# Performance work log

Measured on AMD Instinct MI355X. Metric: run time of the kernel, lower is better.

The kernel has to match this reference:

```python
import jax, jax.numpy as jnp
import numpy as np

TOPK = 5
EPS = 1e-8  # torch CosineSimilarity eps


def setup_inputs() -> dict:
    key = jax.random.key(0)
    k1, k2, k3 = jax.random.split(key, 3)
    B, N, D, L = 64, 100000, 768, 32
    query = jax.random.normal(k1, (B, D), dtype=jnp.float32)
    knowledge_embed = jax.random.normal(k2, (N, D), dtype=jnp.float32)
    knowledge_full = jax.random.randint(k3, (N, L), 0, 30000, dtype=jnp.int32)
    return {"query": query, "knowledge_embed": knowledge_embed, "knowledge_full": knowledge_full}


def reference(query, knowledge_embed, knowledge_full):
    # Batched cosine similarity: [B, N]
    q_norm = jnp.linalg.norm(query, axis=-1, keepdims=True)            # [B, 1]
    k_norm = jnp.linalg.norm(knowledge_embed, axis=-1, keepdims=True)  # [N, 1]
    dots = jnp.einsum("bd,nd->bn", query, knowledge_embed)             # [B, N]
    denom = jnp.maximum(q_norm * k_norm.T, EPS)                        # [B, N]
    sims = dots / denom
    # topk over knowledge axis
    _, indices = jax.lax.top_k(sims, TOPK)                             # [B, topk]
    topk_embed = knowledge_embed[indices]                              # [B, topk, D]
    topk_knowledge = knowledge_full[indices]                           # [B, topk, L]
    return (topk_knowledge, topk_embed)
```

## Files before the change

kernel.cpp:

```cpp
#include <hip/hip_runtime.h>
#include <cfloat>
#include <climits>


#define BQ 64
#define DD 768
#define NK 100000
#define LK 32
#define K_TOP 5
#define TROWS 16
#define NTIL (NK / TROWS)
#define NBLKS 512
#define T_CAND 16

typedef __attribute__((ext_vector_type(8))) short short8;
typedef __attribute__((ext_vector_type(4))) float f32x4;

static __device__ __forceinline__ ushort bf16_rtn(float x) {
    uint u = __float_as_uint(x);
    return (ushort)((u + 0x7FFFu + ((u >> 16) & 1u)) >> 16);
}

#define INS8(v, n, va, ia)                                                  \
    _Pragma("unroll")                                                       \
    for (int m_ = 0; m_ < 8; ++m_) {                                        \
        if ((v) > va[m_]) {                                                 \
            float tv_ = va[m_]; va[m_] = (v); (v) = tv_;                    \
            int ti_ = ia[m_]; ia[m_] = (n); (n) = ti_;                      \
        }                                                                   \
    }

__global__ __launch_bounds__(256) void prep_kernel(const float* __restrict__ q,
                                                   ushort* __restrict__ qf,
                                                   float* __restrict__ qn) {
    const int b = blockIdx.x, t = threadIdx.x;
    __shared__ float red[4];
    float v[3];
    float s = 0.f;
#pragma unroll
    for (int i = 0; i < 3; ++i) {
        v[i] = q[b * DD + t + i * 256];
        s = fmaf(v[i], v[i], s);
    }
    for (int off = 32; off > 0; off >>= 1) s += __shfl_down(s, off, 64);
    if ((t & 63) == 0) red[t >> 6] = s;
    __syncthreads();
    const float tot = red[0] + red[1] + red[2] + red[3];
    const float rq = rsqrtf(tot);
    const int qb = b >> 4, bi = b & 15;
#pragma unroll
    for (int i = 0; i < 3; ++i) {
        const int k = t + i * 256;
        const int kt = k >> 5, lg = (k >> 3) & 3, j = k & 7;
        qf[((size_t)(kt * 4 + qb) * 64 + lg * 16 + bi) * 8 + j] = bf16_rtn(v[i] * rq);
    }
    if (t == 0) qn[b] = sqrtf(tot);
}

__global__ __launch_bounds__(256) void sims_kernel(const ushort* __restrict__ qf,
                                                   const float* __restrict__ ke,
                                                   float2* __restrict__ pv) {
    __shared__ ushort Bb[2][TROWS * DD];
    __shared__ float  S[BQ][17];

    const int t = threadIdx.x;
    const int w = t >> 6, l = t & 63;
    const int lg = l >> 4, li = l & 15;
    const int qd = t & 63, jq = t >> 6;

    float v8[8]; int i8[8];
#pragma unroll
    for (int m = 0; m < 8; ++m) { v8[m] = -FLT_MAX; i8[m] = INT_MAX; }

    f32x4 sr[4][3];
    int tile = blockIdx.x;

    {
        const float* g = ke + (size_t)(tile * TROWS + w * 4) * DD + l * 4;
#pragma unroll
        for (int i = 0; i < 4; ++i)
#pragma unroll
            for (int c = 0; c < 3; ++c)
                sr[i][c] = *(const f32x4*)(g + i * DD + c * 256);
    }

    int cur = 0;
    while (true) {
        const int nxt = tile + NBLKS;

        char* bb = (char*)(&Bb[cur][0]);
#pragma unroll
        for (int i = 0; i < 4; ++i) {
            float s = 0.f;
#pragma unroll
            for (int c = 0; c < 3; ++c)
#pragma unroll
                for (int j = 0; j < 4; ++j) s = fmaf(sr[i][c][j], sr[i][c][j], s);
#pragma unroll
            for (int off = 1; off < 64; off <<= 1) s += __shfl_xor(s, off, 64);
            const float rk = rsqrtf(s);
            const int row = w * 4 + i;
            const int base = row * 1536 + l * 8;
            const int sw = (row & 7) << 4;
#pragma unroll
            for (int c = 0; c < 3; ++c) {
                ushort4 u = make_ushort4(bf16_rtn(sr[i][c][0] * rk),
                                         bf16_rtn(sr[i][c][1] * rk),
                                         bf16_rtn(sr[i][c][2] * rk),
                                         bf16_rtn(sr[i][c][3] * rk));
                *(ushort4*)(bb + ((base + c * 512) ^ sw)) = u;
            }
        }
        if (nxt < NTIL) {
            const float* g = ke + (size_t)(nxt * TROWS + w * 4) * DD + l * 4;
#pragma unroll
            for (int i = 0; i < 4; ++i)
#pragma unroll
                for (int c = 0; c < 3; ++c)
                    sr[i][c] = *(const f32x4*)(g + i * DD + c * 256);
        }
        asm volatile("s_waitcnt lgkmcnt(0)" ::: "memory");
        __builtin_amdgcn_sched_barrier(0);
        __builtin_amdgcn_s_barrier();
        __builtin_amdgcn_sched_barrier(0);

        const ushort* aq = qf + (size_t)w * 512 + l * 8;
        const int boff = li * 1536 + lg * 16;
        const int bsw = (li & 7) << 4;
        f32x4 acc = (f32x4){0.f, 0.f, 0.f, 0.f};
        short8 a[4], br[2];
        a[0] = *(const short8*)(aq);
        a[1] = *(const short8*)(aq + 2048);
        a[2] = *(const short8*)(aq + 4096);
        br[0] = *(const short8*)(bb + (boff ^ bsw));
#pragma unroll
        for (int kt = 0; kt < 24; ++kt) {
            const int ca = kt & 3, cb = kt & 1;
            if (kt < 21) a[(kt + 3) & 3] = *(const short8*)(aq + (kt + 3) * 2048);
            if (kt < 23)
                br[cb ^ 1] = *(const short8*)(bb + ((boff + (kt + 1) * 64) ^ bsw));
            acc = __builtin_amdgcn_mfma_f32_16x16x32_bf16(a[ca], br[cb], acc, 0, 0, 0);
        }

#pragma unroll
        for (int r = 0; r < 4; ++r) S[w * 16 + lg * 4 + r][li] = acc[r];
        asm volatile("s_waitcnt lgkmcnt(0)" ::: "memory");
        __builtin_amdgcn_sched_barrier(0);
        __builtin_amdgcn_s_barrier();
        __builtin_amdgcn_sched_barrier(0);

        {
            const int nb = tile * TROWS + jq * 4;
#pragma unroll
            for (int j = 0; j < 4; ++j) {
                float v = S[qd][jq * 4 + j]; int n = nb + j;
                INS8(v, n, v8, i8);
            }
        }
        if (nxt >= NTIL) break;
        tile = nxt; cur ^= 1;
    }

    __syncthreads();
    float2* mg = (float2*)(&Bb[0][0]);
#pragma unroll
    for (int m = 0; m < 8; ++m) mg[t * 8 + m] = make_float2(v8[m], __int_as_float(i8[m]));
    __syncthreads();
    if (t < BQ) {
        float vf[8]; int nf[8];
#pragma unroll
        for (int m = 0; m < 8; ++m) { vf[m] = -FLT_MAX; nf[m] = INT_MAX; }
        for (int s = 0; s < 4; ++s) {
            const float2* rowp = &mg[(t + s * 64) * 8];
#pragma unroll
            for (int m = 0; m < 8; ++m) {
                float v = rowp[m].x; int n = __float_as_int(rowp[m].y);
                INS8(v, n, vf, nf);
            }
        }
        float2* dst = pv + ((size_t)t * NBLKS + blockIdx.x) * 8;
#pragma unroll
        for (int m = 0; m < 8; ++m) dst[m] = make_float2(vf[m], __int_as_float(nf[m]));
    }
}

__global__ __launch_bounds__(256) void merge_rescore_kernel(
    const float2* __restrict__ pv,
    const float* __restrict__ q, const float* __restrict__ ke,
    const int* __restrict__ kf, const float* __restrict__ qn,
    float* __restrict__ out) {
    const int qi = blockIdx.x, t = threadIdx.x;
    __shared__ float sv[256][8];
    __shared__ int   si[256][8];
    __shared__ int   ci[T_CAND];
    __shared__ float cs_[T_CAND];
    __shared__ int   fi[K_TOP];

    float v8[8]; int i8[8];
#pragma unroll
    for (int m = 0; m < 8; ++m) { v8[m] = -FLT_MAX; i8[m] = INT_MAX; }

    const float2* src = pv + (size_t)qi * NBLKS * 8;
#pragma unroll 4
    for (int c = t; c < NBLKS * 8; c += 256) {
        float2 e = src[c];
        float v = e.x; int n = __float_as_int(e.y);
        INS8(v, n, v8, i8);
    }
#pragma unroll
    for (int m = 0; m < 8; ++m) { sv[t][m] = v8[m]; si[t][m] = i8[m]; }
    __syncthreads();

    for (int active = 64; active >= 4; active >>= 2) {
        if (t < active) {
#pragma unroll
            for (int m = 0; m < 8; ++m) { v8[m] = -FLT_MAX; i8[m] = INT_MAX; }
            for (int s = 0; s < 4; ++s) {
                int row = t * 4 + s;
#pragma unroll
                for (int m = 0; m < 8; ++m) {
                    float v = sv[row][m]; int n = si[row][m];
                    INS8(v, n, v8, i8);
                }
            }
        }
        __syncthreads();
        if (t < active) {
#pragma unroll
            for (int m = 0; m < 8; ++m) { sv[t][m] = v8[m]; si[t][m] = i8[m]; }
        }
        __syncthreads();
    }

    if (t == 0) {
        float v16[T_CAND]; int i16[T_CAND];
#pragma unroll
        for (int m = 0; m < T_CAND; ++m) { v16[m] = -FLT_MAX; i16[m] = INT_MAX; }
        for (int row = 0; row < 4; ++row) {
#pragma unroll
            for (int m = 0; m < 8; ++m) {
                float v = sv[row][m]; int n = si[row][m];
#pragma unroll
                for (int p = 0; p < T_CAND; ++p) {
                    if (v > v16[p]) {
                        float tv = v16[p]; v16[p] = v; v = tv;
                        int ti = i16[p]; i16[p] = n; n = ti;
                    }
                }
            }
        }
#pragma unroll
        for (int m = 0; m < T_CAND; ++m) ci[m] = i16[m];
    }
    __syncthreads();

    {
        const int w = t >> 6, lane = t & 63;
        for (int cc = 0; cc < 4; ++cc) {
            int c = w * 4 + cc;
            int row = ci[c];
            const float* kp = ke + (size_t)row * DD + lane * 12;
            const float* qp = q + qi * DD + lane * 12;
            float d = 0.f, ks = 0.f;
#pragma unroll
            for (int i = 0; i < 12; ++i) {
                float kv = kp[i];
                d = fmaf(qp[i], kv, d);
                ks = fmaf(kv, kv, ks);
            }
#pragma unroll
            for (int off = 32; off > 0; off >>= 1) {
                d += __shfl_xor(d, off, 64);
                ks += __shfl_xor(ks, off, 64);
            }
            if (lane == 0)
                cs_[c] = d / fmaxf(qn[qi] * sqrtf(ks), 1e-8f);
        }
    }
    __syncthreads();

    if (t == 0) {
        float v5[K_TOP]; int i5[K_TOP];
#pragma unroll
        for (int m = 0; m < K_TOP; ++m) { v5[m] = -FLT_MAX; i5[m] = INT_MAX; }
        for (int c = 0; c < T_CAND; ++c) {
            float v = cs_[c]; int n = ci[c];
#pragma unroll
            for (int m = 0; m < K_TOP; ++m) {
                bool take = (v > v5[m]) || (v == v5[m] && n < i5[m]);
                if (take) {
                    float tv = v5[m]; v5[m] = v; v = tv;
                    int ti = i5[m]; i5[m] = n; n = ti;
                }
            }
        }
#pragma unroll
        for (int m = 0; m < K_TOP; ++m) fi[m] = i5[m];
    }
    __syncthreads();

    for (int pos = t; pos < K_TOP * LK; pos += 256) {
        int m = pos >> 5, lgi = pos & 31;
        out[(qi * K_TOP + m) * LK + lgi] = (float)kf[(size_t)fi[m] * LK + lgi];
    }
    const int EO = BQ * K_TOP * LK;
    for (int m = 0; m < K_TOP; ++m) {
        const float4* srcp = (const float4*)(ke + (size_t)fi[m] * DD);
        float4* dstp = (float4*)(out + EO + (size_t)(qi * K_TOP + m) * DD);
        for (int pos = t; pos < DD / 4; pos += 256) dstp[pos] = srcp[pos];
    }
}

extern "C" void kernel_launch(void* const* d_in, const int* in_sizes, int n_in,
                              void* d_out, int out_size, void* d_ws, size_t ws_size,
                              hipStream_t stream) {
    const float* query = (const float*)d_in[0];
    const float* ke    = (const float*)d_in[1];
    const int*   kf    = (const int*)d_in[2];
    float* out = (float*)d_out;

    float2* pv = (float2*)d_ws;
    ushort* qf = (ushort*)((char*)d_ws + (size_t)BQ * NBLKS * 8 * sizeof(float2));
    float*  qn = (float*)((char*)qf + (size_t)24 * 4 * 64 * 8 * sizeof(ushort));

    prep_kernel<<<BQ, 256, 0, stream>>>(query, qf, qn);
    sims_kernel<<<NBLKS, 256, 0, stream>>>(qf, ke, pv);
    merge_rescore_kernel<<<BQ, 256, 0, stream>>>(pv, query, ke, kf, qn, out);
}
```

Baseline: 172.2 us.

## Give each wave its own key tile, converting to bf16 in registers without LDS staging

The sims kernel now assigns one 16-row key tile to each wavefront instead of one per block. Each wave loads fp32 key rows straight into registers, packs them to bf16 by truncation with a byte permute, and accumulates the squared norm as it goes, so the LDS double buffer and the block barriers disappear. The query is stored row-major in bf16 and read from global/L2 per wave, and the grid grows to 768 blocks. The cost is more query reloads from global memory and truncating rather than round-to-nearest bf16 conversion for keys, which the rescore stage has to absorb.

```diff
diff --git a/kernel.cpp b/kernel.cpp
--- a/kernel.cpp
+++ b/kernel.cpp
@@ -10,7 +10,8 @@
 #define K_TOP 5
 #define TROWS 16
 #define NTIL (NK / TROWS)
-#define NBLKS 512
+#define NBLK 768
+#define NWAV (NBLK * 4)
 #define T_CAND 16
 
 typedef __attribute__((ext_vector_type(8))) short short8;
@@ -31,7 +32,7 @@
     }
 
 __global__ __launch_bounds__(256) void prep_kernel(const float* __restrict__ q,
-                                                   ushort* __restrict__ qf,
+                                                   ushort* __restrict__ qbf,
                                                    float* __restrict__ qn) {
     const int b = blockIdx.x, t = threadIdx.x;
     __shared__ float red[4];
@@ -47,122 +48,99 @@
     __syncthreads();
     const float tot = red[0] + red[1] + red[2] + red[3];
     const float rq = rsqrtf(tot);
-    const int qb = b >> 4, bi = b & 15;
-#pragma unroll
-    for (int i = 0; i < 3; ++i) {
-        const int k = t + i * 256;
-        const int kt = k >> 5, lg = (k >> 3) & 3, j = k & 7;
-        qf[((size_t)(kt * 4 + qb) * 64 + lg * 16 + bi) * 8 + j] = bf16_rtn(v[i] * rq);
-    }
+#pragma unroll
+    for (int i = 0; i < 3; ++i)
+        qbf[b * DD + t + i * 256] = bf16_rtn(v[i] * rq);
     if (t == 0) qn[b] = sqrtf(tot);
 }
 
-__global__ __launch_bounds__(256) void sims_kernel(const ushort* __restrict__ qf,
+__global__ __launch_bounds__(256) void sims_kernel(const ushort* __restrict__ qbf,
                                                    const float* __restrict__ ke,
                                                    float2* __restrict__ pv) {
-    __shared__ ushort Bb[2][TROWS * DD];
-    __shared__ float  S[BQ][17];
+    __shared__ float  S[4][BQ][17];
+    __shared__ float2 mg[256 * 8];
 
     const int t = threadIdx.x;
     const int w = t >> 6, l = t & 63;
     const int lg = l >> 4, li = l & 15;
-    const int qd = t & 63, jq = t >> 6;
 
     float v8[8]; int i8[8];
 #pragma unroll
     for (int m = 0; m < 8; ++m) { v8[m] = -FLT_MAX; i8[m] = INT_MAX; }
 
-    f32x4 sr[4][3];
-    int tile = blockIdx.x;
-
-    {
-        const float* g = ke + (size_t)(tile * TROWS + w * 4) * DD + l * 4;
-#pragma unroll
-        for (int i = 0; i < 4; ++i)
-#pragma unroll
-            for (int c = 0; c < 3; ++c)
-                sr[i][c] = *(const f32x4*)(g + i * DD + c * 256);
-    }
-
-    int cur = 0;
-    while (true) {
-        const int nxt = tile + NBLKS;
-
-        char* bb = (char*)(&Bb[cur][0]);
-#pragma unroll
-        for (int i = 0; i < 4; ++i) {
-            float s = 0.f;
-#pragma unroll
-            for (int c = 0; c < 3; ++c)
-#pragma unroll
-                for (int j = 0; j < 4; ++j) s = fmaf(sr[i][c][j], sr[i][c][j], s);
-#pragma unroll
-            for (int off = 1; off < 64; off <<= 1) s += __shfl_xor(s, off, 64);
-            const float rk = rsqrtf(s);
-            const int row = w * 4 + i;
-            const int base = row * 1536 + l * 8;
-            const int sw = (row & 7) << 4;
-#pragma unroll
-            for (int c = 0; c < 3; ++c) {
-                ushort4 u = make_ushort4(bf16_rtn(sr[i][c][0] * rk),
-                                         bf16_rtn(sr[i][c][1] * rk),
-                                         bf16_rtn(sr[i][c][2] * rk),
-                                         bf16_rtn(sr[i][c][3] * rk));
-                *(ushort4*)(bb + ((base + c * 512) ^ sw)) = u;
-            }
-        }
-        if (nxt < NTIL) {
-            const float* g = ke + (size_t)(nxt * TROWS + w * 4) * DD + l * 4;
-#pragma unroll
-            for (int i = 0; i < 4; ++i)
-#pragma unroll
-                for (int c = 0; c < 3; ++c)
-                    sr[i][c] = *(const f32x4*)(g + i * DD + c * 256);
-        }
-        asm volatile("s_waitcnt lgkmcnt(0)" ::: "memory");
-        __builtin_amdgcn_sched_barrier(0);
-        __builtin_amdgcn_s_barrier();
-        __builtin_amdgcn_sched_barrier(0);
-
-        const ushort* aq = qf + (size_t)w * 512 + l * 8;
-        const int boff = li * 1536 + lg * 16;
-        const int bsw = (li & 7) << 4;
-        f32x4 acc = (f32x4){0.f, 0.f, 0.f, 0.f};
-        short8 a[4], br[2];
-        a[0] = *(const short8*)(aq);
-        a[1] = *(const short8*)(aq + 2048);
-        a[2] = *(const short8*)(aq + 4096);
-        br[0] = *(const short8*)(bb + (boff ^ bsw));
+    const ushort* abase = qbf + (size_t)li * DD + lg * 8;
+
+    const int gw = blockIdx.x * 4 + w;
+    for (int tile = gw; tile < NTIL; tile += NWAV) {
+        const int n0 = tile * TROWS;
+        const float* bbase = ke + (size_t)(n0 + li) * DD + lg * 8;
+
+        f32x4  br[4][2];
+        short8 ar[2][4];
+
+#pragma unroll
+        for (int p = 0; p < 4; ++p) {
+            br[p][0] = *(const f32x4*)(bbase + p * 32);
+            br[p][1] = *(const f32x4*)(bbase + p * 32 + 4);
+        }
+#pragma unroll
+        for (int s = 0; s < 2; ++s)
+#pragma unroll
+            for (int g = 0; g < 4; ++g)
+                ar[s][g] = *(const short8*)(abase + (size_t)g * 16 * DD + s * 32);
+
+        f32x4 acc[4];
+#pragma unroll
+        for (int g = 0; g < 4; ++g) acc[g] = (f32x4){0.f, 0.f, 0.f, 0.f};
+        float bsq = 0.f;
+
 #pragma unroll
         for (int kt = 0; kt < 24; ++kt) {
-            const int ca = kt & 3, cb = kt & 1;
-            if (kt < 21) a[(kt + 3) & 3] = *(const short8*)(aq + (kt + 3) * 2048);
-            if (kt < 23)
-                br[cb ^ 1] = *(const short8*)(bb + ((boff + (kt + 1) * 64) ^ bsw));
-            acc = __builtin_amdgcn_mfma_f32_16x16x32_bf16(a[ca], br[cb], acc, 0, 0, 0);
-        }
-
-#pragma unroll
-        for (int r = 0; r < 4; ++r) S[w * 16 + lg * 4 + r][li] = acc[r];
-        asm volatile("s_waitcnt lgkmcnt(0)" ::: "memory");
-        __builtin_amdgcn_sched_barrier(0);
-        __builtin_amdgcn_s_barrier();
-        __builtin_amdgcn_sched_barrier(0);
-
-        {
-            const int nb = tile * TROWS + jq * 4;
-#pragma unroll
-            for (int j = 0; j < 4; ++j) {
-                float v = S[qd][jq * 4 + j]; int n = nb + j;
-                INS8(v, n, v8, i8);
-            }
-        }
-        if (nxt >= NTIL) break;
-        tile = nxt; cur ^= 1;
-    }
-
-    __syncthreads();
-    float2* mg = (float2*)(&Bb[0][0]);
+            const int cb = kt & 3, ca = kt & 1;
+            union { short8 s8; uint u[4]; } pk;
+#pragma unroll
+            for (int p = 0; p < 4; ++p) {
+                float f0 = br[cb][p >> 1][(p & 1) * 2 + 0];
+                float f1 = br[cb][p >> 1][(p & 1) * 2 + 1];
+                bsq = fmaf(f0, f0, bsq);
+                bsq = fmaf(f1, f1, bsq);
+                pk.u[p] = __builtin_amdgcn_perm(__float_as_uint(f1),
+                                                __float_as_uint(f0), 0x07060302u);
+            }
+#pragma unroll
+            for (int g = 0; g < 4; ++g)
+                acc[g] = __builtin_amdgcn_mfma_f32_16x16x32_bf16(
+                    ar[ca][g], pk.s8, acc[g], 0, 0, 0);
+            if (kt < 20) {
+                br[cb][0] = *(const f32x4*)(bbase + (kt + 4) * 32);
+                br[cb][1] = *(const f32x4*)(bbase + (kt + 4) * 32 + 4);
+            }
+            if (kt < 22) {
+#pragma unroll
+                for (int g = 0; g < 4; ++g)
+                    ar[ca][g] = *(const short8*)(abase + (size_t)g * 16 * DD
+                                                 + (kt + 2) * 32);
+            }
+        }
+
+        bsq += __shfl_xor(bsq, 16, 64);
+        bsq += __shfl_xor(bsq, 32, 64);
+        const float rk = rsqrtf(bsq);
+
+#pragma unroll
+        for (int g = 0; g < 4; ++g)
+#pragma unroll
+            for (int r = 0; r < 4; ++r)
+                S[w][g * 16 + lg * 4 + r][li] = acc[g][r] * rk;
+#pragma unroll
+        for (int j = 0; j < TROWS; ++j) {
+            float v = S[w][l][j];
+            int n = n0 + j;
+            INS8(v, n, v8, i8);
+        }
+    }
+
+    __syncthreads();
 #pragma unroll
     for (int m = 0; m < 8; ++m) mg[t * 8 + m] = make_float2(v8[m], __int_as_float(i8[m]));
     __syncthreads();
@@ -178,7 +156,7 @@
                 INS8(v, n, vf, nf);
             }
         }
-        float2* dst = pv + ((size_t)t * NBLKS + blockIdx.x) * 8;
+        float2* dst = pv + ((size_t)t * NBLK + blockIdx.x) * 8;
 #pragma unroll
         for (int m = 0; m < 8; ++m) dst[m] = make_float2(vf[m], __int_as_float(nf[m]));
     }
@@ -200,9 +178,8 @@
 #pragma unroll
     for (int m = 0; m < 8; ++m) { v8[m] = -FLT_MAX; i8[m] = INT_MAX; }
 
-    const float2* src = pv + (size_t)qi * NBLKS * 8;
-#pragma unroll 4
-    for (int c = t; c < NBLKS * 8; c += 256) {
+    const float2* src = pv + (size_t)qi * NBLK * 8;
+    for (int c = t; c < NBLK * 8; c += 256) {
         float2 e = src[c];
         float v = e.x; int n = __float_as_int(e.y);
         INS8(v, n, v8, i8);
@@ -319,11 +296,11 @@
     const int*   kf    = (const int*)d_in[2];
     float* out = (float*)d_out;
 
-    float2* pv = (float2*)d_ws;
-    ushort* qf = (ushort*)((char*)d_ws + (size_t)BQ * NBLKS * 8 * sizeof(float2));
-    float*  qn = (float*)((char*)qf + (size_t)24 * 4 * 64 * 8 * sizeof(ushort));
-
-    prep_kernel<<<BQ, 256, 0, stream>>>(query, qf, qn);
-    sims_kernel<<<NBLKS, 256, 0, stream>>>(qf, ke, pv);
+    float2* pv  = (float2*)d_ws;
+    ushort* qbf = (ushort*)((char*)d_ws + (size_t)BQ * NBLK * 8 * sizeof(float2));
+    float*  qn  = (float*)((char*)qbf + (size_t)BQ * DD * sizeof(ushort));
+
+    prep_kernel<<<BQ, 256, 0, stream>>>(query, qbf, qn);
+    sims_kernel<<<NBLK, 256, 0, stream>>>(qbf, ke, pv);
     merge_rescore_kernel<<<BQ, 256, 0, stream>>>(pv, query, ke, kf, qn, out);
 }
```

Result: slower. 226.1 us (+31.3%).
